# Optimization experiments

Hardware: AMD Instinct MI355X
Metric: run time of the kernel (lower is better)

## Reference

```python
import jax, jax.numpy as jnp
import numpy as np

B, T, E, H = 2, 2048, 1024, 16
D = E // H  # head dim = 64
ROPE_BASE = 10000.0


def setup_inputs() -> dict:
    key = jax.random.key(0)
    k0, k1, k2 = jax.random.split(key, 3)
    s = 0.02  # GPT-style init scale
    return {
        "x": jax.random.normal(k0, (B, T, E), jnp.float32),
        "w_qkv": jax.random.normal(k1, (E, 3 * E), jnp.float32) * s,
        "b_qkv": jnp.zeros((3 * E,), jnp.float32),
        "w_out": jax.random.normal(k2, (E, E), jnp.float32) * s,
        "b_out": jnp.zeros((E,), jnp.float32),
    }


def _rope_tables(t, d, dtype):
    # Llama rotary with scale=1 (YaRN degenerates to vanilla RoPE)
    inv_freq = 1.0 / (ROPE_BASE ** (jnp.arange(0, d, 2, dtype=jnp.float32) / d))
    freqs = jnp.arange(t, dtype=jnp.float32)[:, None] * inv_freq[None, :]  # [T, D/2]
    emb = jnp.concatenate([freqs, freqs], axis=-1)  # [T, D]
    return jnp.cos(emb).astype(dtype), jnp.sin(emb).astype(dtype)


def _rotate_half(x):
    return jnp.concatenate([-x[..., D // 2:], x[..., : D // 2]], axis=-1)


def reference(x, w_qkv, b_qkv, w_out, b_out):
    # 1) fused QKV projection
    qkv = x @ w_qkv + b_qkv                      # [B, T, 3E]
    q, k, v = jnp.split(qkv, 3, axis=-1)

    def heads(t):
        return t.reshape(B, T, H, D).transpose(0, 2, 1, 3)  # [B, H, T, D]

    q, k, v = heads(q), heads(k), heads(v)

    # 2) rotary position embedding on q, k
    cos, sin = _rope_tables(T, D, x.dtype)       # [T, D], broadcasts over B, H
    q = q * cos + _rotate_half(q) * sin
    k = k * cos + _rotate_half(k) * sin

    # 3) causal scaled dot-product attention
    scale = jnp.asarray(1.0 / np.sqrt(D), x.dtype)
    scores = jnp.einsum("bhqd,bhkd->bhqk", q, k) * scale
    causal = jnp.tril(jnp.ones((T, T), dtype=bool))
    scores = jnp.where(causal, scores, jnp.finfo(scores.dtype).min)
    attn = jax.nn.softmax(scores, axis=-1)
    out = jnp.einsum("bhqk,bhkd->bhqd", attn, v)  # [B, H, T, D]

    # 4) merge heads + output projection
    out = out.transpose(0, 2, 1, 3).reshape(B, T, E)
    return out @ w_out + b_out
```

## Files before the change

### kernel.cpp

```cpp
#include <hip/hip_runtime.h>
#include <hip/hip_bf16.h>
#include <stdint.h>

#define B_  2
#define T_  2048
#define E_  1024
#define H_  16
#define D_  64
#define BH_ 32

typedef unsigned short ushort_t;
typedef __attribute__((ext_vector_type(8))) short bfrag;
typedef __attribute__((ext_vector_type(4))) short s16x4;
typedef __attribute__((ext_vector_type(4))) float f32x4;

__device__ __forceinline__ ushort_t f2b(float f) {
    uint32_t u = __builtin_bit_cast(uint32_t, f);
    u += 0x7fffu + ((u >> 16) & 1u);
    return (ushort_t)(u >> 16);
}

#if defined(__has_builtin)
#if __has_builtin(__builtin_amdgcn_exp2f)
#define EXP2(x) __builtin_amdgcn_exp2f(x)
#endif
#endif
#ifndef EXP2
__device__ __forceinline__ float hexp2_(float x) {
    float r;
    asm volatile("v_exp_f32 %0, %1\n\ts_nop 1" : "=v"(r) : "v"(x));
    return r;
}
#define EXP2(x) hexp2_(x)
#endif

__device__ __forceinline__ uint32_t cvtpk_bf16(float lo, float hi) {
    uint32_t r;
    asm("v_cvt_pk_bf16_f32 %0, %1, %2" : "=v"(r) : "v"(lo), "v"(hi));
    return r;
}

typedef const __attribute__((address_space(1))) uint8_t* gas_t;
typedef __attribute__((address_space(3))) uint8_t* las_t;
__device__ __forceinline__ void gload_lds16(const void* g, void* l) {
    __builtin_amdgcn_global_load_lds((gas_t)g, (las_t)l, 16, 0, 0);
}
__device__ __forceinline__ void drain_vmem() {
    asm volatile("s_waitcnt vmcnt(0)" ::: "memory");
    __builtin_amdgcn_sched_barrier(0);
}

__global__ __launch_bounds__(256) void prep_kernel(const float* __restrict__ x, const float* __restrict__ w_qkv,
                                                   const float* __restrict__ w_out, ushort_t* __restrict__ xb,
                                                   ushort_t* __restrict__ wqkvT, ushort_t* __restrict__ woutT,
                                                   float2* __restrict__ cstab) {
    __shared__ float tile[32][33];
    int blk = blockIdx.x, tid = threadIdx.x;
    if (blk < 256) {
        int id = blk * 256 + tid;
        int j = id & 31, t = id >> 5;
        float ang = (float)t * expf(-(float)j * 0.2878231366242558f);
        float s, c;
        sincosf(ang, &s, &c);
        cstab[id] = make_float2(c, s);
    } else if (blk < 2304) {
        int i = ((blk - 256) * 256 + tid) * 8;
        float4 a = *(const float4*)(x + i);
        float4 b = *(const float4*)(x + i + 4);
        ushort_t r[8] = {f2b(a.x), f2b(a.y), f2b(a.z), f2b(a.w), f2b(b.x), f2b(b.y), f2b(b.z), f2b(b.w)};
        *(uint4*)(xb + i) = *(const uint4*)r;
    } else {
        const float* in;
        ushort_t* out;
        int R, C, bx, by;
        if (blk < 5376) { in = w_qkv; out = wqkvT; R = 1024; C = 3072; int t = blk - 2304; bx = t % 96; by = t / 96; }
        else            { in = w_out; out = woutT; R = 1024; C = 1024; int t = blk - 5376; bx = t % 32; by = t / 32; }
        int tx = tid & 31, ty = tid >> 5;
        int c0 = bx * 32, r0 = by * 32;
#pragma unroll
        for (int i = 0; i < 4; ++i)
            tile[ty + i * 8][tx] = in[(size_t)(r0 + ty + i * 8) * C + c0 + tx];
        __syncthreads();
#pragma unroll
        for (int i = 0; i < 4; ++i)
            out[(size_t)(c0 + ty + i * 8) * R + r0 + tx] = f2b(tile[tx][ty + i * 8]);
    }
}

__global__ __launch_bounds__(256) void gemm_qkv_kernel(const ushort_t* __restrict__ A, const ushort_t* __restrict__ Bt,
                                                       const float* __restrict__ bias, const float2* __restrict__ cstab,
                                                       ushort_t* __restrict__ qw, ushort_t* __restrict__ kw,
                                                       ushort_t* __restrict__ vw) {
    const int K = 1024;
    __shared__ ushort_t As[2][128 * 64];
    __shared__ ushort_t Bs[2][128 * 64];
    int tid = threadIdx.x, lane = tid & 63, wid = tid >> 6;
    int lm = lane & 15, lg = lane >> 4;
    int bid = blockIdx.x;
    int xcd = bid & 7, idx = bid >> 3;
    int bm = xcd * 4 + idx / 24;
    int bn = idx % 24;
    int wm = wid >> 1, wn = wid & 1;

    int cbase = bn * 128 + wn * 64;
    bool qk = (cbase < 2048);

    f32x4 acc[4][4] = {};
    const ushort_t* ag = A + (size_t)bm * 128 * K;
    const ushort_t* bg = Bt + (size_t)bn * 128 * K;

#define QKV_STAGE(kt_, buf_)                                                              \
    _Pragma("unroll")                                                                     \
    for (int c = 0; c < 4; ++c) {                                                         \
        int G = c * 256 + tid;                                                            \
        int rr = G >> 3;                                                                  \
        int gs = (G & 7) ^ (rr & 7);                                                      \
        gload_lds16(ag + (size_t)rr * K + (kt_) * 64 + gs * 8, &As[buf_][(c * 256 + wid * 64) * 8]); \
        gload_lds16(bg + (size_t)rr * K + (kt_) * 64 + gs * 8, &Bs[buf_][(c * 256 + wid * 64) * 8]); \
    }

    int cur = 0;
    QKV_STAGE(0, 0);
    drain_vmem();
    __syncthreads();

    for (int kt = 0; kt < K / 64; ++kt) {
        if (kt + 1 < K / 64) { QKV_STAGE(kt + 1, cur ^ 1); }
        bfrag a[2][4], b[2][4];
#pragma unroll
        for (int kk = 0; kk < 2; ++kk) {
#pragma unroll
            for (int mi = 0; mi < 4; ++mi) {
                int row = wm * 64 + mi * 16 + lm;
                int slot = (kk * 4 + lg) ^ (lm & 7);
                a[kk][mi] = *(const bfrag*)&As[cur][row * 64 + slot * 8];
            }
#pragma unroll
            for (int ni = 0; ni < 4; ++ni) {
                int row = wn * 64 + ni * 16 + lm;
                int slot = (kk * 4 + lg) ^ (lm & 7);
                b[kk][ni] = *(const bfrag*)&Bs[cur][row * 64 + slot * 8];
            }
        }
        if (qk) {
#pragma unroll
            for (int kk = 0; kk < 2; ++kk)
#pragma unroll
                for (int mi = 0; mi < 4; ++mi)
#pragma unroll
                    for (int ni = 0; ni < 4; ++ni)
                        acc[mi][ni] = __builtin_amdgcn_mfma_f32_16x16x32_bf16(b[kk][ni], a[kk][mi], acc[mi][ni], 0, 0, 0);
        } else {
#pragma unroll
            for (int kk = 0; kk < 2; ++kk)
#pragma unroll
                for (int mi = 0; mi < 4; ++mi)
#pragma unroll
                    for (int ni = 0; ni < 4; ++ni)
                        acc[mi][ni] = __builtin_amdgcn_mfma_f32_16x16x32_bf16(a[kk][mi], b[kk][ni], acc[mi][ni], 0, 0, 0);
        }
        drain_vmem();
        __syncthreads();
        cur ^= 1;
    }
#undef QKV_STAGE

    int sel = cbase >> 10;
    int h = (cbase & 1023) >> 6;
    if (qk) {
        ushort_t* dst = sel ? kw : qw;
        float scale = sel ? 1.0f : 0.18033688011112042f;
        float4 bias4[4];
#pragma unroll
        for (int ni = 0; ni < 4; ++ni)
            bias4[ni] = *(const float4*)&bias[cbase + ni * 16 + lg * 4];
#pragma unroll
        for (int mi = 0; mi < 4; ++mi) {
            int r = bm * 128 + wm * 64 + mi * 16 + lm;
            int bb = r >> 11, t = r & (T_ - 1);
            size_t rowbase = ((size_t)(bb * H_ + h) * T_ + t) * D_;
#pragma unroll
            for (int nip = 0; nip < 2; ++nip) {
                const float4* cs2 = (const float4*)(cstab + t * 32 + nip * 16 + lg * 4);
                float4 ca = cs2[0], cb = cs2[1];
                float xl[4], xh[4];
#pragma unroll
                for (int i = 0; i < 4; ++i) {
                    xl[i] = acc[mi][nip][i]     + ((const float*)&bias4[nip])[i];
                    xh[i] = acc[mi][nip + 2][i] + ((const float*)&bias4[nip + 2])[i];
                }
                float rl0 = (xl[0] * ca.x - xh[0] * ca.y) * scale;
                float rl1 = (xl[1] * ca.z - xh[1] * ca.w) * scale;
                float rl2 = (xl[2] * cb.x - xh[2] * cb.y) * scale;
                float rl3 = (xl[3] * cb.z - xh[3] * cb.w) * scale;
                float rh0 = (xh[0] * ca.x + xl[0] * ca.y) * scale;
                float rh1 = (xh[1] * ca.z + xl[1] * ca.w) * scale;
                float rh2 = (xh[2] * cb.x + xl[2] * cb.y) * scale;
                float rh3 = (xh[3] * cb.z + xl[3] * cb.w) * scale;
                uint2 wlo, whi;
                wlo.x = cvtpk_bf16(rl0, rl1); wlo.y = cvtpk_bf16(rl2, rl3);
                whi.x = cvtpk_bf16(rh0, rh1); whi.y = cvtpk_bf16(rh2, rh3);
                *(uint2*)&dst[rowbase + nip * 16 + lg * 4]      = wlo;
                *(uint2*)&dst[rowbase + 32 + nip * 16 + lg * 4] = whi;
            }
        }
    } else {
        float bb4[4];
#pragma unroll
        for (int ni = 0; ni < 4; ++ni) bb4[ni] = bias[cbase + ni * 16 + lm];
#pragma unroll
        for (int ni = 0; ni < 4; ++ni) {
            int d = ni * 16 + lm;
#pragma unroll
            for (int mi = 0; mi < 4; ++mi) {
                int r = bm * 128 + wm * 64 + mi * 16 + lg * 4;
                int bb = r >> 11, tq = r & (T_ - 1);
                uint2 w;
                w.x = cvtpk_bf16(acc[mi][ni][0] + bb4[ni], acc[mi][ni][1] + bb4[ni]);
                w.y = cvtpk_bf16(acc[mi][ni][2] + bb4[ni], acc[mi][ni][3] + bb4[ni]);
                *(uint2*)&vw[((size_t)(bb * H_ + h) * D_ + d) * T_ + tq] = w;
            }
        }
    }
}

__device__ __forceinline__ void stage_tile(const ushort_t* __restrict__ kb, const ushort_t* __restrict__ vb,
                                           ushort_t* kdst, ushort_t* vdst, int k0, int wid, int lane) {
#pragma unroll
    for (int c = 0; c < 2; ++c) {
        int G = (c * 4 + wid) * 64 + lane;
        int rr = G >> 3;
        int gs = (G & 7) ^ (rr & 7);
        gload_lds16(kb + (size_t)(k0 + rr) * D_ + gs * 8, kdst + (c * 4 + wid) * 512);
        gload_lds16(vb + (size_t)rr * T_ + k0 + gs * 8, vdst + (c * 4 + wid) * 512);
    }
}

__global__ __launch_bounds__(256, 2) void flash_kernel(const ushort_t* __restrict__ q, const ushort_t* __restrict__ k,
                                                       const ushort_t* __restrict__ vt, ushort_t* __restrict__ o) {
    __shared__ ushort_t smem[2][4096];
    int tid = threadIdx.x, lane = tid & 63, wid = tid >> 6;
    int lm = lane & 15, lg = lane >> 4;
    int x = blockIdx.x & 7, r = blockIdx.x >> 3;
    int half = r >> 5, idx = r & 31;
    int bh = x * 4 + (idx & 3);
    int jq = idx >> 2;
    int j = half ? jq : 15 - jq;
    int q0w = j * 128 + wid * 32;
    int b = bh >> 4, h = bh & 15;
    int nt = 2 * j + 2;

    const ushort_t* qb = q + (size_t)bh * T_ * D_;
    const ushort_t* kb = k + (size_t)bh * T_ * D_;
    const ushort_t* vb = vt + (size_t)bh * D_ * T_;

    bfrag aq[2][2];
#pragma unroll
    for (int s = 0; s < 2; ++s)
#pragma unroll
        for (int hh = 0; hh < 2; ++hh)
            aq[s][hh] = *(const bfrag*)(qb + (size_t)(q0w + s * 16 + lm) * D_ + hh * 32 + lg * 8);

    f32x4 acc[2][4] = {};
    float lsum[2] = {0.f, 0.f};

    for (int t = 0; t < nt; ++t) {
        int k0 = t * 64;
        __syncthreads();
        stage_tile(kb, vb, smem[0], smem[1], k0, wid, lane);
        drain_vmem();
        __syncthreads();

        if (k0 <= q0w + 31) {
            bfrag ka[4][2];
#pragma unroll
            for (int sb = 0; sb < 4; ++sb)
#pragma unroll
                for (int hh = 0; hh < 2; ++hh) {
                    int rr = sb * 16 + lm;
                    int gr = (hh * 4 + lg) ^ (rr & 7);
                    ka[sb][hh] = *(const bfrag*)&smem[0][rr * 64 + gr * 8];
                }
            s16x4 vq[4][4];
#pragma unroll
            for (int qq = 0; qq < 4; ++qq)
#pragma unroll
                for (int db = 0; db < 4; ++db) {
                    int rr = db * 16 + lm;
                    int gr = (qq * 2 + (lg >> 1)) ^ (rr & 7);
                    vq[qq][db] = *(const s16x4*)&smem[1][rr * 64 + gr * 8 + (lg & 1) * 4];
                }
            f32x4 st[2][4];
#pragma unroll
            for (int s = 0; s < 2; ++s)
#pragma unroll
                for (int sb = 0; sb < 4; ++sb) {
                    f32x4 z = {};
                    z = __builtin_amdgcn_mfma_f32_16x16x32_bf16(ka[sb][0], aq[s][0], z, 0, 0, 0);
                    st[s][sb] = __builtin_amdgcn_mfma_f32_16x16x32_bf16(ka[sb][1], aq[s][1], z, 0, 0, 0);
                }
            if (k0 + 63 > q0w) {
#pragma unroll
                for (int s = 0; s < 2; ++s)
#pragma unroll
                    for (int sb = 0; sb < 4; ++sb)
#pragma unroll
                        for (int i = 0; i < 4; ++i)
                            if (k0 + sb * 16 + lg * 4 + i > q0w + s * 16 + lm) st[s][sb][i] = -1e30f;
            }
#pragma unroll
            for (int s = 0; s < 2; ++s) {
                float pv[4][4];
#pragma unroll
                for (int sb = 0; sb < 4; ++sb)
#pragma unroll
                    for (int i = 0; i < 4; ++i)
                        pv[sb][i] = EXP2(st[s][sb][i]);
                lsum[s] += ((pv[0][0] + pv[0][1]) + (pv[0][2] + pv[0][3])) +
                           ((pv[1][0] + pv[1][1]) + (pv[1][2] + pv[1][3])) +
                           ((pv[2][0] + pv[2][1]) + (pv[2][2] + pv[2][3])) +
                           ((pv[3][0] + pv[3][1]) + (pv[3][2] + pv[3][3]));
                uint4 u0, u1;
                u0.x = cvtpk_bf16(pv[0][0], pv[0][1]);
                u0.y = cvtpk_bf16(pv[0][2], pv[0][3]);
                u0.z = cvtpk_bf16(pv[1][0], pv[1][1]);
                u0.w = cvtpk_bf16(pv[1][2], pv[1][3]);
                u1.x = cvtpk_bf16(pv[2][0], pv[2][1]);
                u1.y = cvtpk_bf16(pv[2][2], pv[2][3]);
                u1.z = cvtpk_bf16(pv[3][0], pv[3][1]);
                u1.w = cvtpk_bf16(pv[3][2], pv[3][3]);
                bfrag pf0 = __builtin_bit_cast(bfrag, u0);
                bfrag pf1 = __builtin_bit_cast(bfrag, u1);
#pragma unroll
                for (int db = 0; db < 4; ++db) {
                    bfrag va01 = __builtin_shufflevector(vq[0][db], vq[1][db], 0, 1, 2, 3, 4, 5, 6, 7);
                    bfrag va23 = __builtin_shufflevector(vq[2][db], vq[3][db], 0, 1, 2, 3, 4, 5, 6, 7);
                    acc[s][db] = __builtin_amdgcn_mfma_f32_16x16x32_bf16(va01, pf0, acc[s][db], 0, 0, 0);
                    acc[s][db] = __builtin_amdgcn_mfma_f32_16x16x32_bf16(va23, pf1, acc[s][db], 0, 0, 0);
                }
            }
        }
    }

#pragma unroll
    for (int s = 0; s < 2; ++s) {
        float lM = lsum[s];
        lM += __shfl_xor(lM, 16);
        lM += __shfl_xor(lM, 32);
        float inv = 1.0f / lM;
        int tq = q0w + s * 16 + lm;
        size_t ro = ((size_t)b * T_ + tq) * E_ + h * D_;
#pragma unroll
        for (int db = 0; db < 4; ++db) {
            uint2 w;
            w.x = cvtpk_bf16(acc[s][db][0] * inv, acc[s][db][1] * inv);
            w.y = cvtpk_bf16(acc[s][db][2] * inv, acc[s][db][3] * inv);
            *(uint2*)(o + ro + db * 16 + lg * 4) = w;
        }
    }
}

__global__ __launch_bounds__(256) void gemm_out_kernel(const ushort_t* __restrict__ A, const ushort_t* __restrict__ Bt,
                                                       const float* __restrict__ bias, float* __restrict__ out) {
    const int K = 1024;
    __shared__ ushort_t As[2][128 * 64];
    __shared__ ushort_t Bs[2][64 * 64];
    int tid = threadIdx.x, lane = tid & 63, wid = tid >> 6;
    int lm = lane & 15, lg = lane >> 4;
    int bid = blockIdx.x;
    int xcd = bid & 7, idx = bid >> 3;
    int bm = xcd * 4 + idx / 16;
    int bn = idx % 16;

    f32x4 acc[2][4] = {};
    const ushort_t* ag = A + (size_t)bm * 128 * K;
    const ushort_t* bg = Bt + (size_t)bn * 64 * K;

#define OUT_STAGE(kt_, buf_)                                                              \
    _Pragma("unroll")                                                                     \
    for (int c = 0; c < 4; ++c) {                                                         \
        int G = c * 256 + tid;                                                            \
        int rr = G >> 3;                                                                  \
        int gs = (G & 7) ^ (rr & 7);                                                      \
        gload_lds16(ag + (size_t)rr * K + (kt_) * 64 + gs * 8, &As[buf_][(c * 256 + wid * 64) * 8]); \
    }                                                                                     \
    _Pragma("unroll")                                                                     \
    for (int c = 0; c < 2; ++c) {                                                         \
        int G = c * 256 + tid;                                                            \
        int rr = G >> 3;                                                                  \
        int gs = (G & 7) ^ (rr & 7);                                                      \
        gload_lds16(bg + (size_t)rr * K + (kt_) * 64 + gs * 8, &Bs[buf_][(c * 256 + wid * 64) * 8]); \
    }

    int cur = 0;
    OUT_STAGE(0, 0);
    drain_vmem();
    __syncthreads();

    for (int kt = 0; kt < K / 64; ++kt) {
        if (kt + 1 < K / 64) { OUT_STAGE(kt + 1, cur ^ 1); }
        bfrag a[2][2], b[2][4];
#pragma unroll
        for (int kk = 0; kk < 2; ++kk) {
#pragma unroll
            for (int mi = 0; mi < 2; ++mi) {
                int row = wid * 32 + mi * 16 + lm;
                int slot = (kk * 4 + lg) ^ (lm & 7);
                a[kk][mi] = *(const bfrag*)&As[cur][row * 64 + slot * 8];
            }
#pragma unroll
            for (int ni = 0; ni < 4; ++ni) {
                int row = ni * 16 + lm;
                int slot = (kk * 4 + lg) ^ (lm & 7);
                b[kk][ni] = *(const bfrag*)&Bs[cur][row * 64 + slot * 8];
            }
        }
#pragma unroll
        for (int kk = 0; kk < 2; ++kk)
#pragma unroll
            for (int mi = 0; mi < 2; ++mi)
#pragma unroll
                for (int ni = 0; ni < 4; ++ni)
                    acc[mi][ni] = __builtin_amdgcn_mfma_f32_16x16x32_bf16(a[kk][mi], b[kk][ni], acc[mi][ni], 0, 0, 0);
        drain_vmem();
        __syncthreads();
        cur ^= 1;
    }
#undef OUT_STAGE

#pragma unroll
    for (int ni = 0; ni < 4; ++ni) {
        int c = bn * 64 + ni * 16 + lm;
        float bb = bias[c];
#pragma unroll
        for (int mi = 0; mi < 2; ++mi) {
#pragma unroll
            for (int i = 0; i < 4; ++i) {
                int r = bm * 128 + wid * 32 + mi * 16 + lg * 4 + i;
                out[(size_t)r * 1024 + c] = acc[mi][ni][i] + bb;
            }
        }
    }
}

extern "C" void kernel_launch(void* const* d_in, const int* in_sizes, int n_in,
                              void* d_out, int out_size, void* d_ws, size_t ws_size,
                              hipStream_t stream) {
    const float* x     = (const float*)d_in[0];
    const float* w_qkv = (const float*)d_in[1];
    const float* b_qkv = (const float*)d_in[2];
    const float* w_out = (const float*)d_in[3];
    const float* b_out = (const float*)d_in[4];
    float* out = (float*)d_out;

    ushort_t* ws    = (ushort_t*)d_ws;
    ushort_t* xb    = ws;
    ushort_t* wqkvT = xb + 4194304;
    ushort_t* woutT = wqkvT + 3145728;
    ushort_t* qw    = woutT + 1048576;
    ushort_t* kw    = qw + 4194304;
    ushort_t* vw    = kw + 4194304;
    ushort_t* ao    = vw + 4194304;
    float2*   cstab = (float2*)(ao + 4194304);

    prep_kernel<<<dim3(6400), 256, 0, stream>>>(x, w_qkv, w_out, xb, wqkvT, woutT, cstab);
    gemm_qkv_kernel<<<dim3(768), 256, 0, stream>>>(xb, wqkvT, b_qkv, cstab, qw, kw, vw);
    flash_kernel<<<dim3(512), 256, 0, stream>>>(qw, kw, vw, ao);
    gemm_out_kernel<<<dim3(512), 256, 0, stream>>>(ao, woutT, b_out, out);
}
```

Measured before the change: 113.2 us.

## Restructure QKV GEMM into 256x256 tiles with 8-wave phased pipeline

```diff
diff --git a/kernel.cpp b/kernel.cpp
--- a/kernel.cpp
+++ b/kernel.cpp
@@ -87,83 +87,102 @@
     }
 }
 
-__global__ __launch_bounds__(256) void gemm_qkv_kernel(const ushort_t* __restrict__ A, const ushort_t* __restrict__ Bt,
+__global__ __launch_bounds__(512) void gemm_qkv_kernel(const ushort_t* __restrict__ A, const ushort_t* __restrict__ Bt,
                                                        const float* __restrict__ bias, const float2* __restrict__ cstab,
                                                        ushort_t* __restrict__ qw, ushort_t* __restrict__ kw,
                                                        ushort_t* __restrict__ vw) {
     const int K = 1024;
-    __shared__ ushort_t As[2][128 * 64];
-    __shared__ ushort_t Bs[2][128 * 64];
+    __shared__ ushort_t As[2][256 * 64];
+    __shared__ ushort_t Bs[2][256 * 64];
     int tid = threadIdx.x, lane = tid & 63, wid = tid >> 6;
     int lm = lane & 15, lg = lane >> 4;
     int bid = blockIdx.x;
     int xcd = bid & 7, idx = bid >> 3;
-    int bm = xcd * 4 + idx / 24;
-    int bn = idx % 24;
-    int wm = wid >> 1, wn = wid & 1;
-
-    int cbase = bn * 128 + wn * 64;
-    bool qk = (cbase < 2048);
-
-    f32x4 acc[4][4] = {};
-    const ushort_t* ag = A + (size_t)bm * 128 * K;
-    const ushort_t* bg = Bt + (size_t)bn * 128 * K;
-
-#define QKV_STAGE(kt_, buf_)                                                              \
-    _Pragma("unroll")                                                                     \
-    for (int c = 0; c < 4; ++c) {                                                         \
-        int G = c * 256 + tid;                                                            \
-        int rr = G >> 3;                                                                  \
-        int gs = (G & 7) ^ (rr & 7);                                                      \
-        gload_lds16(ag + (size_t)rr * K + (kt_) * 64 + gs * 8, &As[buf_][(c * 256 + wid * 64) * 8]); \
-        gload_lds16(bg + (size_t)rr * K + (kt_) * 64 + gs * 8, &Bs[buf_][(c * 256 + wid * 64) * 8]); \
-    }
-
-    int cur = 0;
-    QKV_STAGE(0, 0);
-    drain_vmem();
-    __syncthreads();
-
-    for (int kt = 0; kt < K / 64; ++kt) {
-        if (kt + 1 < K / 64) { QKV_STAGE(kt + 1, cur ^ 1); }
-        bfrag a[2][4], b[2][4];
-#pragma unroll
-        for (int kk = 0; kk < 2; ++kk) {
-#pragma unroll
-            for (int mi = 0; mi < 4; ++mi) {
-                int row = wm * 64 + mi * 16 + lm;
-                int slot = (kk * 4 + lg) ^ (lm & 7);
-                a[kk][mi] = *(const bfrag*)&As[cur][row * 64 + slot * 8];
-            }
-#pragma unroll
-            for (int ni = 0; ni < 4; ++ni) {
-                int row = wn * 64 + ni * 16 + lm;
-                int slot = (kk * 4 + lg) ^ (lm & 7);
-                b[kk][ni] = *(const bfrag*)&Bs[cur][row * 64 + slot * 8];
-            }
-        }
-        if (qk) {
-#pragma unroll
-            for (int kk = 0; kk < 2; ++kk)
-#pragma unroll
-                for (int mi = 0; mi < 4; ++mi)
-#pragma unroll
-                    for (int ni = 0; ni < 4; ++ni)
-                        acc[mi][ni] = __builtin_amdgcn_mfma_f32_16x16x32_bf16(b[kk][ni], a[kk][mi], acc[mi][ni], 0, 0, 0);
-        } else {
-#pragma unroll
-            for (int kk = 0; kk < 2; ++kk)
-#pragma unroll
-                for (int mi = 0; mi < 4; ++mi)
-#pragma unroll
-                    for (int ni = 0; ni < 4; ++ni)
-                        acc[mi][ni] = __builtin_amdgcn_mfma_f32_16x16x32_bf16(a[kk][mi], b[kk][ni], acc[mi][ni], 0, 0, 0);
-        }
-        drain_vmem();
-        __syncthreads();
-        cur ^= 1;
-    }
-#undef QKV_STAGE
+    int bm = xcd * 2 + idx / 12;
+    int bn = idx % 12;
+    int wm = wid >> 2, wn = wid & 3;
+    bool qk = (bn < 8);
+    int cbase = bn * 256 + wn * 64;
+    const ushort_t* ag = A + (size_t)bm * 256 * K;
+    const ushort_t* bg = Bt + (size_t)bn * 256 * K;
+    int s_rl = tid >> 3, s_g = tid & 7;
+
+    f32x4 acc[8][4] = {};
+    bfrag a[4], b[4];
+
+#define STQ(SRC, DST, kt_, q_) do { int rr_ = (q_) * 64 + s_rl;                               \
+        gload_lds16(SRC + (size_t)rr_ * K + (kt_) * 64 + ((s_g ^ (rr_ & 7)) * 8),             \
+                    &DST[((q_) * 512 + wid * 64) * 8]); } while (0)
+#define LOADA(bi_, mq_, kk_) { _Pragma("unroll") for (int f = 0; f < 4; ++f) {                \
+        int rA_ = wm * 128 + (mq_) * 64 + f * 16 + lm;                                        \
+        a[f] = *(const bfrag*)&As[bi_][rA_ * 64 + (((kk_) * 4 + lg) ^ (lm & 7)) * 8]; } }
+#define LOADB(bi_, kk_) { _Pragma("unroll") for (int f = 0; f < 4; ++f) {                     \
+        int rB_ = wn * 64 + f * 16 + lm;                                                      \
+        b[f] = *(const bfrag*)&Bs[bi_][rB_ * 64 + (((kk_) * 4 + lg) ^ (lm & 7)) * 8]; } }
+#define DOMFMA(mq_) { if (qk) { _Pragma("unroll") for (int fm = 0; fm < 4; ++fm)              \
+            _Pragma("unroll") for (int fn = 0; fn < 4; ++fn)                                  \
+                acc[(mq_) * 4 + fm][fn] = __builtin_amdgcn_mfma_f32_16x16x32_bf16(            \
+                    b[fn], a[fm], acc[(mq_) * 4 + fm][fn], 0, 0, 0);                          \
+        } else { _Pragma("unroll") for (int fm = 0; fm < 4; ++fm)                             \
+            _Pragma("unroll") for (int fn = 0; fn < 4; ++fn)                                  \
+                acc[(mq_) * 4 + fm][fn] = __builtin_amdgcn_mfma_f32_16x16x32_bf16(            \
+                    a[fm], b[fn], acc[(mq_) * 4 + fm][fn], 0, 0, 0); } }
+#define MIDSYNC { __builtin_amdgcn_s_barrier();                                               \
+        asm volatile("s_waitcnt lgkmcnt(0)" ::: "memory");                                    \
+        __builtin_amdgcn_sched_barrier(0); __builtin_amdgcn_s_setprio(1); }
+#define ENDPHASE { __builtin_amdgcn_s_setprio(0); __builtin_amdgcn_s_barrier(); }
+#define ENDCHK { __builtin_amdgcn_s_setprio(0);                                               \
+        asm volatile("s_waitcnt vmcnt(2)" ::: "memory");                                      \
+        __builtin_amdgcn_sched_barrier(0); __builtin_amdgcn_s_barrier(); }
+#define ENDCHK0 { __builtin_amdgcn_s_setprio(0);                                              \
+        asm volatile("s_waitcnt vmcnt(0)" ::: "memory");                                      \
+        __builtin_amdgcn_sched_barrier(0); __builtin_amdgcn_s_barrier(); }
+
+    STQ(ag, As[0], 0, 0); STQ(ag, As[0], 0, 1); STQ(ag, As[0], 0, 2); STQ(ag, As[0], 0, 3);
+    STQ(bg, Bs[0], 0, 0); STQ(bg, Bs[0], 0, 1); STQ(bg, Bs[0], 0, 2); STQ(bg, Bs[0], 0, 3);
+    STQ(ag, As[1], 1, 0); STQ(ag, As[1], 1, 2);
+    asm volatile("s_waitcnt vmcnt(2)" ::: "memory");
+    __builtin_amdgcn_sched_barrier(0);
+    __builtin_amdgcn_s_barrier();
+
+    for (int i = 0; i < 8; ++i) {
+        int c1 = 2 * i + 1, t2 = 2 * i + 2, t3 = 2 * i + 3;
+        bool st2 = (t2 < 16), st3 = (t3 < 16);
+        STQ(ag, As[1], c1, 1); STQ(ag, As[1], c1, 3);
+        LOADA(0, 0, 0); LOADB(0, 0);
+        MIDSYNC; DOMFMA(0); ENDPHASE;
+        STQ(bg, Bs[1], c1, 0); STQ(bg, Bs[1], c1, 1);
+        LOADA(0, 1, 0);
+        MIDSYNC; DOMFMA(1); ENDPHASE;
+        STQ(bg, Bs[1], c1, 2); STQ(bg, Bs[1], c1, 3);
+        LOADA(0, 0, 1); LOADB(0, 1);
+        MIDSYNC; DOMFMA(0); ENDPHASE;
+        if (st2) { STQ(ag, As[0], t2, 0); STQ(ag, As[0], t2, 2); }
+        LOADA(0, 1, 1);
+        MIDSYNC; DOMFMA(1);
+        if (st2) ENDCHK else ENDCHK0;
+        if (st2) { STQ(ag, As[0], t2, 1); STQ(ag, As[0], t2, 3); }
+        LOADA(1, 0, 0); LOADB(1, 0);
+        MIDSYNC; DOMFMA(0); ENDPHASE;
+        if (st2) { STQ(bg, Bs[0], t2, 0); STQ(bg, Bs[0], t2, 1); }
+        LOADA(1, 1, 0);
+        MIDSYNC; DOMFMA(1); ENDPHASE;
+        if (st2) { STQ(bg, Bs[0], t2, 2); STQ(bg, Bs[0], t2, 3); }
+        LOADA(1, 0, 1); LOADB(1, 1);
+        MIDSYNC; DOMFMA(0); ENDPHASE;
+        if (st3) { STQ(ag, As[1], t3, 0); STQ(ag, As[1], t3, 2); }
+        LOADA(1, 1, 1);
+        MIDSYNC; DOMFMA(1);
+        if (st2) ENDCHK else ENDCHK0;
+    }
+#undef STQ
+#undef LOADA
+#undef LOADB
+#undef DOMFMA
+#undef MIDSYNC
+#undef ENDPHASE
+#undef ENDCHK
+#undef ENDCHK0
 
     int sel = cbase >> 10;
     int h = (cbase & 1023) >> 6;
@@ -175,8 +194,8 @@
         for (int ni = 0; ni < 4; ++ni)
             bias4[ni] = *(const float4*)&bias[cbase + ni * 16 + lg * 4];
 #pragma unroll
-        for (int mi = 0; mi < 4; ++mi) {
-            int r = bm * 128 + wm * 64 + mi * 16 + lm;
+        for (int mi = 0; mi < 8; ++mi) {
+            int r = bm * 256 + wm * 128 + (mi >> 2) * 64 + (mi & 3) * 16 + lm;
             int bb = r >> 11, t = r & (T_ - 1);
             size_t rowbase = ((size_t)(bb * H_ + h) * T_ + t) * D_;
 #pragma unroll
@@ -185,9 +204,9 @@
                 float4 ca = cs2[0], cb = cs2[1];
                 float xl[4], xh[4];
 #pragma unroll
-                for (int i = 0; i < 4; ++i) {
-                    xl[i] = acc[mi][nip][i]     + ((const float*)&bias4[nip])[i];
-                    xh[i] = acc[mi][nip + 2][i] + ((const float*)&bias4[nip + 2])[i];
+                for (int i2 = 0; i2 < 4; ++i2) {
+                    xl[i2] = acc[mi][nip][i2]     + ((const float*)&bias4[nip])[i2];
+                    xh[i2] = acc[mi][nip + 2][i2] + ((const float*)&bias4[nip + 2])[i2];
                 }
                 float rl0 = (xl[0] * ca.x - xh[0] * ca.y) * scale;
                 float rl1 = (xl[1] * ca.z - xh[1] * ca.w) * scale;
@@ -212,8 +231,8 @@
         for (int ni = 0; ni < 4; ++ni) {
             int d = ni * 16 + lm;
 #pragma unroll
-            for (int mi = 0; mi < 4; ++mi) {
-                int r = bm * 128 + wm * 64 + mi * 16 + lg * 4;
+            for (int mi = 0; mi < 8; ++mi) {
+                int r = bm * 256 + wm * 128 + (mi >> 2) * 64 + (mi & 3) * 16 + lg * 4;
                 int bb = r >> 11, tq = r & (T_ - 1);
                 uint2 w;
                 w.x = cvtpk_bf16(acc[mi][ni][0] + bb4[ni], acc[mi][ni][1] + bb4[ni]);
@@ -464,7 +483,7 @@
     float2*   cstab = (float2*)(ao + 4194304);
 
     prep_kernel<<<dim3(6400), 256, 0, stream>>>(x, w_qkv, w_out, xb, wqkvT, woutT, cstab);
-    gemm_qkv_kernel<<<dim3(768), 256, 0, stream>>>(xb, wqkvT, b_qkv, cstab, qw, kw, vw);
+    gemm_qkv_kernel<<<dim3(192), 512, 0, stream>>>(xb, wqkvT, b_qkv, cstab, qw, kw, vw);
     flash_kernel<<<dim3(512), 256, 0, stream>>>(qw, kw, vw, ao);
     gemm_out_kernel<<<dim3(512), 256, 0, stream>>>(ao, woutT, b_out, out);
 }
```

New measurement: 164.0 us. 44.8% more time.
